# Kernel tuning notes

Measured on AMD Instinct MI355X. Metric: run time of the kernel, lower is better.

The kernel has to match this reference:

```python
import jax, jax.numpy as jnp
import numpy as np
from jax import lax

DIL_R = 2            # dilation_radius
K = 2 * DIL_R + 1    # 5x5 morphology kernel
FOCAL_ALPHA = 0.25
FOCAL_GAMMA = 2.0
BOUNDARY_W = 1.0
IGNORE_IDX = 250


def setup_inputs() -> dict:
    key = jax.random.key(0)
    k1, k2 = jax.random.split(key)
    pred = jax.random.normal(k1, (32, 2, 512, 512), dtype=jnp.float32)
    target = jax.random.randint(k2, (32, 512, 512), 0, 2, dtype=jnp.int64)
    return {"pred": pred, "target": target}


def _boundary_mask(target):
    # labels float, 5x5 all-ones conv with 'same' padding (zero pad),
    # dilated = (conv > 0), eroded = (-conv(-x) > K*K-1) == (conv(x) > K*K-1)
    x = target.astype(jnp.float32)[:, None]                    # [B,1,H,W]
    kern = jnp.ones((1, 1, K, K), dtype=jnp.float32)
    s = lax.conv_general_dilated(x, kern, (1, 1), 'SAME',
                                 dimension_numbers=('NCHW', 'OIHW', 'NCHW'))
    dilated = (s > 0).astype(jnp.float32)
    eroded = (s > (K * K - 1)).astype(jnp.float32)
    return (dilated - eroded)[:, 0]                            # [B,H,W]


def _loss(pred, target, boundary):
    logp = jax.nn.log_softmax(pred, axis=1)                    # [B,2,H,W]
    # per-pixel CE
    ce_pix = -jnp.take_along_axis(logp, target[:, None].astype(jnp.int32), axis=1)[:, 0]  # [B,H,W]
    # main CE with ignore_index=250
    valid = (target != IGNORE_IDX)
    ce_loss = jnp.sum(ce_pix * valid) / jnp.maximum(jnp.sum(valid), 1)
    # focal loss (no ignore, mean over all pixels)
    pt = jnp.exp(-ce_pix)
    focal = jnp.mean(FOCAL_ALPHA * (1.0 - pt) ** FOCAL_GAMMA * ce_pix)
    # boundary dice on class-1 prob
    prob1 = jnp.exp(logp[:, 1])                                # softmax(pred,1)[:,1]
    tgt_f = target.astype(jnp.float32)
    bp = prob1 * boundary
    bt = tgt_f * boundary
    inter = jnp.sum(bp * bt, axis=(1, 2))
    union = jnp.sum(bp, axis=(1, 2)) + jnp.sum(bt, axis=(1, 2))
    dice = 2.0 * inter / (union + 1e-8)
    bdice = 1.0 - jnp.mean(dice)
    return ce_loss + BOUNDARY_W * focal + BOUNDARY_W * bdice


def reference(pred, target):
    boundary = _boundary_mask(target)
    return _loss(pred, target, boundary)
```

## Files before the change

### kernel.cpp

```cpp
#include <hip/hip_runtime.h>
#include <math.h>

#define BATCH 32
#define HH 512
#define WW 512
#define TH 16
#define HALO 2
#define SRH (TH + 2*HALO)
#define NDW (WW / 4)
#define CSTRIDE 132
#define NPIX ((float)BATCH * HH * WW)
#define HW (HH * WW)
#define NBLK (BATCH * (HH / TH))


__global__ __launch_bounds__(256, 4) void bel_main_kernel(
        const float* __restrict__ pred,
        const int*   __restrict__ target,
        float*       __restrict__ ws) {
    __shared__ unsigned int t8[SRH][NDW];
    __shared__ unsigned int csum[TH][CSTRIDE];
    __shared__ float red[6][4];

    const int tid = threadIdx.x;
    const int bid = blockIdx.x;
    const int b   = bid >> 5;
    const int ty  = bid & 31;
    const int y0  = ty * TH;
    const size_t tb = (size_t)b * HW;

    if (tid < 2 * TH) {
        int rr = tid >> 1;
        csum[rr][(tid & 1) ? (NDW + 1) : 0] = 0u;
    }

    #pragma unroll
    for (int it = 0; it < (SRH * NDW) / 256; ++it) {
        const int i  = tid + 256 * it;
        const int r  = i >> 7;
        const int c4 = i & 127;
        const int gy = y0 - HALO + r;
        unsigned int packed = 0u;
        if ((unsigned)gy < (unsigned)HH) {
            const int4 v = *(const int4*)(target + tb + ((size_t)gy << 9) + (c4 << 2));
            packed = (unsigned)v.x | ((unsigned)v.y << 8)
                   | ((unsigned)v.z << 16) | ((unsigned)v.w << 24);
        }
        t8[r][c4] = packed;
    }
    __syncthreads();

    #pragma unroll
    for (int it = 0; it < (TH * NDW) / 256; ++it) {
        const int j = tid + 256 * it;
        const int r = j >> 7;
        const int c = j & 127;
        csum[r][c + 1] = t8[r][c] + t8[r+1][c] + t8[r+2][c]
                       + t8[r+3][c] + t8[r+4][c];
    }
    __syncthreads();

    const float4* __restrict__ pr0 = (const float4*)(pred + tb * 2);
    const float4* __restrict__ pr1 = (const float4*)(pred + tb * 2 + HW);
    const int base4 = (y0 << 7) + tid;

    float4 F0[8], F1[8];
    #pragma unroll
    for (int it = 0; it < 8; ++it) F0[it] = pr0[base4 + 256 * it];
    #pragma unroll
    for (int it = 0; it < 8; ++it) F1[it] = pr1[base4 + 256 * it];

    float ce_acc = 0.f, cnt_acc = 0.f, focal_acc = 0.f;
    float inter_acc = 0.f, bp_acc = 0.f, bt_acc = 0.f;

    const unsigned long long M5 = 0xFFFFFFFFFFull;
    const unsigned long long ALL5 = 0x0505050505ull;

    const int g  = tid & 127;
    const int rb = tid >> 7;

    #pragma unroll
    for (int it = 0; it < 8; ++it) {
        const int r = rb + 2 * it;

        const float4 f0 = F0[it];
        const float4 f1 = F1[it];

        const unsigned int L = csum[r][g];
        const unsigned int M = csum[r][g + 1];
        const unsigned int R = csum[r][g + 2];
        const unsigned int tdw = t8[r + HALO][g];

        const unsigned long long lo  = (unsigned long long)L | ((unsigned long long)M << 32);
        const unsigned long long mid = (unsigned long long)M | ((unsigned long long)R << 32);

        #pragma unroll
        for (int i = 0; i < 4; ++i) {
            unsigned long long w;
            if      (i == 0) w = (lo  >> 16) & M5;
            else if (i == 1) w = (lo  >> 24) & M5;
            else if (i == 2) w =  mid        & M5;
            else             w = (mid >>  8) & M5;
            const float bm = (w != 0ull && w != ALL5) ? 1.0f : 0.0f;

            const unsigned int tv = (tdw >> (8 * i)) & 0xFFu;

            const float p0 = (i == 0) ? f0.x : (i == 1) ? f0.y : (i == 2) ? f0.z : f0.w;
            const float p1 = (i == 0) ? f1.x : (i == 1) ? f1.y : (i == 2) ? f1.z : f1.w;

            const float d  = p1 - p0;
            const float e  = __expf(-fabsf(d));
            const float rz = 1.0f / (1.0f + e);
            const float pmin = e * rz;
            const float prob1 = (d >= 0.0f) ? rz : pmin;
            const float pt = tv ? prob1 : (1.0f - prob1);
            const float ce = -__logf(pt);

            const float valid = (tv != 250u) ? 1.0f : 0.0f;
            ce_acc  += ce * valid;
            cnt_acc += valid;

            const float omp = 1.0f - pt;
            focal_acc += omp * omp * ce;

            const float bp = prob1 * bm;
            const float bt = (float)tv * bm;
            inter_acc += bp * bt;
            bp_acc    += bp;
            bt_acc    += bt;
        }
    }

    float vals[6] = {ce_acc, cnt_acc, focal_acc * 0.25f, inter_acc, bp_acc, bt_acc};
    #pragma unroll
    for (int jj = 0; jj < 6; ++jj) {
        float v = vals[jj];
        #pragma unroll
        for (int off = 32; off > 0; off >>= 1)
            v += __shfl_down(v, off, 64);
        vals[jj] = v;
    }
    const int wave = tid >> 6;
    const int lane = tid & 63;
    if (lane == 0) {
        #pragma unroll
        for (int jj = 0; jj < 6; ++jj) red[jj][wave] = vals[jj];
    }
    __syncthreads();
    if (tid == 0) {
        float* p = ws + bid * 8;
        #pragma unroll
        for (int jj = 0; jj < 6; ++jj)
            p[jj] = red[jj][0] + red[jj][1] + red[jj][2] + red[jj][3];
    }
}

__global__ void bel_finalize_kernel(const float* __restrict__ ws,
                                    float* __restrict__ out) {
    __shared__ float simg[BATCH][4];
    const int t = threadIdx.x;
    const int b = t >> 3;
    const int s = t & 7;

    float a0 = 0.f, a1 = 0.f, a2 = 0.f, a3 = 0.f, a4 = 0.f, a5 = 0.f;
    #pragma unroll
    for (int k = 0; k < 4; ++k) {
        const int bid = (b << 5) + s + (k << 3);
        const float* p = ws + bid * 8;
        a0 += p[0]; a1 += p[1]; a2 += p[2];
        a3 += p[3]; a4 += p[4]; a5 += p[5];
    }
    #pragma unroll
    for (int off = 4; off > 0; off >>= 1) {
        a0 += __shfl_down(a0, off, 8);
        a1 += __shfl_down(a1, off, 8);
        a2 += __shfl_down(a2, off, 8);
        a3 += __shfl_down(a3, off, 8);
        a4 += __shfl_down(a4, off, 8);
        a5 += __shfl_down(a5, off, 8);
    }
    if (s == 0) {
        simg[b][0] = a0;
        simg[b][1] = a1;
        simg[b][2] = a2;
        simg[b][3] = 2.0f * a3 / (a4 + a5 + 1e-8f);
    }
    __syncthreads();
    if (t < BATCH) {
        float ce  = simg[t][0];
        float cnt = simg[t][1];
        float foc = simg[t][2];
        float dc  = simg[t][3];
        #pragma unroll
        for (int off = 16; off > 0; off >>= 1) {
            ce  += __shfl_down(ce,  off, 32);
            cnt += __shfl_down(cnt, off, 32);
            foc += __shfl_down(foc, off, 32);
            dc  += __shfl_down(dc,  off, 32);
        }
        if (t == 0) {
            const float ce_loss = ce / fmaxf(cnt, 1.0f);
            const float focal   = foc / NPIX;
            const float bdice   = 1.0f - dc / (float)BATCH;
            out[0] = ce_loss + focal + bdice;
        }
    }
}

extern "C" void kernel_launch(void* const* d_in, const int* in_sizes, int n_in,
                              void* d_out, int out_size, void* d_ws, size_t ws_size,
                              hipStream_t stream) {
    const float* pred   = (const float*)d_in[0];
    const int*   target = (const int*)d_in[1];
    float* ws  = (float*)d_ws;
    float* out = (float*)d_out;

    bel_main_kernel<<<NBLK, 256, 0, stream>>>(pred, target, ws);
    bel_finalize_kernel<<<1, 256, 0, stream>>>(ws, out);
}
```

Before: 117.5 us.

## Split fused kernel into boundary-map pass and prediction-loss pass

```diff
diff --git a/kernel.cpp b/kernel.cpp
--- a/kernel.cpp
+++ b/kernel.cpp
@@ -12,15 +12,15 @@
 #define NPIX ((float)BATCH * HH * WW)
 #define HW (HH * WW)
 #define NBLK (BATCH * (HH / TH))
-
-
-__global__ __launch_bounds__(256, 4) void bel_main_kernel(
-        const float* __restrict__ pred,
-        const int*   __restrict__ target,
-        float*       __restrict__ ws) {
+#define MAP_OFF 16384
+
+
+__global__ __launch_bounds__(256, 4) void bel_boundary_kernel(
+        const int* __restrict__ target,
+        float*     __restrict__ ws) {
     __shared__ unsigned int t8[SRH][NDW];
     __shared__ unsigned int csum[TH][CSTRIDE];
-    __shared__ float red[6][4];
+    __shared__ float red[2][4];
 
     const int tid = threadIdx.x;
     const int bid = blockIdx.x;
@@ -60,31 +60,18 @@
     }
     __syncthreads();
 
-    const float4* __restrict__ pr0 = (const float4*)(pred + tb * 2);
-    const float4* __restrict__ pr1 = (const float4*)(pred + tb * 2 + HW);
-    const int base4 = (y0 << 7) + tid;
-
-    float4 F0[8], F1[8];
-    #pragma unroll
-    for (int it = 0; it < 8; ++it) F0[it] = pr0[base4 + 256 * it];
-    #pragma unroll
-    for (int it = 0; it < 8; ++it) F1[it] = pr1[base4 + 256 * it];
-
-    float ce_acc = 0.f, cnt_acc = 0.f, focal_acc = 0.f;
-    float inter_acc = 0.f, bp_acc = 0.f, bt_acc = 0.f;
-
-    const unsigned long long M5 = 0xFFFFFFFFFFull;
+    unsigned int* __restrict__ mp = (unsigned int*)(ws + MAP_OFF);
+    const int mbase = b * (HW / 4) + (y0 << 7);
+
+    float cnt_acc = 0.f, bt_acc = 0.f;
+    const unsigned long long M5   = 0xFFFFFFFFFFull;
     const unsigned long long ALL5 = 0x0505050505ull;
-
     const int g  = tid & 127;
     const int rb = tid >> 7;
 
     #pragma unroll
     for (int it = 0; it < 8; ++it) {
         const int r = rb + 2 * it;
-
-        const float4 f0 = F0[it];
-        const float4 f1 = F1[it];
 
         const unsigned int L = csum[r][g];
         const unsigned int M = csum[r][g + 1];
@@ -94,6 +81,7 @@
         const unsigned long long lo  = (unsigned long long)L | ((unsigned long long)M << 32);
         const unsigned long long mid = (unsigned long long)M | ((unsigned long long)R << 32);
 
+        unsigned int codedw = 0u;
         #pragma unroll
         for (int i = 0; i < 4; ++i) {
             unsigned long long w;
@@ -101,9 +89,71 @@
             else if (i == 1) w = (lo  >> 24) & M5;
             else if (i == 2) w =  mid        & M5;
             else             w = (mid >>  8) & M5;
-            const float bm = (w != 0ull && w != ALL5) ? 1.0f : 0.0f;
-
+            const unsigned int bm = (w != 0ull && w != ALL5) ? 1u : 0u;
             const unsigned int tv = (tdw >> (8 * i)) & 0xFFu;
+
+            cnt_acc += (tv != 250u) ? 1.0f : 0.0f;
+            bt_acc  += (float)tv * (float)bm;
+
+            codedw |= ((tv & 1u) | (bm << 1)) << (8 * i);
+        }
+        mp[mbase + (r << 7) + g] = codedw;
+    }
+
+    float vals[2] = {cnt_acc, bt_acc};
+    #pragma unroll
+    for (int jj = 0; jj < 2; ++jj) {
+        float v = vals[jj];
+        #pragma unroll
+        for (int off = 32; off > 0; off >>= 1)
+            v += __shfl_down(v, off, 64);
+        vals[jj] = v;
+    }
+    const int wave = tid >> 6;
+    const int lane = tid & 63;
+    if (lane == 0) {
+        red[0][wave] = vals[0];
+        red[1][wave] = vals[1];
+    }
+    __syncthreads();
+    if (tid == 0) {
+        float* p = ws + bid * 16;
+        p[0] = red[0][0] + red[0][1] + red[0][2] + red[0][3];
+        p[1] = red[1][0] + red[1][1] + red[1][2] + red[1][3];
+    }
+}
+
+__global__ __launch_bounds__(256, 4) void bel_pred_kernel(
+        const float* __restrict__ pred,
+        float*       __restrict__ ws) {
+    __shared__ float red[4][4];
+
+    const int tid = threadIdx.x;
+    const int bid = blockIdx.x;
+    const int b   = bid >> 5;
+    const int ty  = bid & 31;
+    const int y0  = ty * TH;
+    const size_t tb = (size_t)b * HW;
+
+    const float4* __restrict__ pr0 = (const float4*)(pred + tb * 2);
+    const float4* __restrict__ pr1 = (const float4*)(pred + tb * 2 + HW);
+    const unsigned int* __restrict__ mp = (const unsigned int*)(ws + MAP_OFF);
+    const int base4 = (y0 << 7) + tid;
+    const int mbase = b * (HW / 4) + base4;
+
+    float ce_acc = 0.f, focal_acc = 0.f, inter_acc = 0.f, bp_acc = 0.f;
+
+    #pragma unroll
+    for (int it = 0; it < 8; ++it) {
+        const float4 f0 = pr0[base4 + 256 * it];
+        const float4 f1 = pr1[base4 + 256 * it];
+        const unsigned int cw = mp[mbase + 256 * it];
+
+        #pragma unroll
+        for (int i = 0; i < 4; ++i) {
+            const unsigned int code = (cw >> (8 * i)) & 0xFFu;
+            const float tv = (float)(code & 1u);
+            const float bm = (float)((code >> 1) & 1u);
 
             const float p0 = (i == 0) ? f0.x : (i == 1) ? f0.y : (i == 2) ? f0.z : f0.w;
             const float p1 = (i == 0) ? f1.x : (i == 1) ? f1.y : (i == 2) ? f1.z : f1.w;
@@ -113,27 +163,22 @@
             const float rz = 1.0f / (1.0f + e);
             const float pmin = e * rz;
             const float prob1 = (d >= 0.0f) ? rz : pmin;
-            const float pt = tv ? prob1 : (1.0f - prob1);
+            const float pt = (code & 1u) ? prob1 : (1.0f - prob1);
             const float ce = -__logf(pt);
 
-            const float valid = (tv != 250u) ? 1.0f : 0.0f;
-            ce_acc  += ce * valid;
-            cnt_acc += valid;
-
+            ce_acc += ce;
             const float omp = 1.0f - pt;
             focal_acc += omp * omp * ce;
 
             const float bp = prob1 * bm;
-            const float bt = (float)tv * bm;
-            inter_acc += bp * bt;
+            inter_acc += bp * tv;
             bp_acc    += bp;
-            bt_acc    += bt;
-        }
-    }
-
-    float vals[6] = {ce_acc, cnt_acc, focal_acc * 0.25f, inter_acc, bp_acc, bt_acc};
-    #pragma unroll
-    for (int jj = 0; jj < 6; ++jj) {
+        }
+    }
+
+    float vals[4] = {ce_acc, focal_acc * 0.25f, inter_acc, bp_acc};
+    #pragma unroll
+    for (int jj = 0; jj < 4; ++jj) {
         float v = vals[jj];
         #pragma unroll
         for (int off = 32; off > 0; off >>= 1)
@@ -144,13 +189,13 @@
     const int lane = tid & 63;
     if (lane == 0) {
         #pragma unroll
-        for (int jj = 0; jj < 6; ++jj) red[jj][wave] = vals[jj];
+        for (int jj = 0; jj < 4; ++jj) red[jj][wave] = vals[jj];
     }
     __syncthreads();
     if (tid == 0) {
-        float* p = ws + bid * 8;
-        #pragma unroll
-        for (int jj = 0; jj < 6; ++jj)
+        float* p = ws + bid * 16 + 8;
+        #pragma unroll
+        for (int jj = 0; jj < 4; ++jj)
             p[jj] = red[jj][0] + red[jj][1] + red[jj][2] + red[jj][3];
     }
 }
@@ -162,46 +207,47 @@
     const int b = t >> 3;
     const int s = t & 7;
 
-    float a0 = 0.f, a1 = 0.f, a2 = 0.f, a3 = 0.f, a4 = 0.f, a5 = 0.f;
+    float cnt = 0.f, bt = 0.f, ce = 0.f, foc = 0.f, inter = 0.f, bp = 0.f;
     #pragma unroll
     for (int k = 0; k < 4; ++k) {
         const int bid = (b << 5) + s + (k << 3);
-        const float* p = ws + bid * 8;
-        a0 += p[0]; a1 += p[1]; a2 += p[2];
-        a3 += p[3]; a4 += p[4]; a5 += p[5];
+        const float* p = ws + bid * 16;
+        cnt += p[0];  bt  += p[1];
+        ce  += p[8];  foc += p[9];
+        inter += p[10]; bp += p[11];
     }
     #pragma unroll
     for (int off = 4; off > 0; off >>= 1) {
-        a0 += __shfl_down(a0, off, 8);
-        a1 += __shfl_down(a1, off, 8);
-        a2 += __shfl_down(a2, off, 8);
-        a3 += __shfl_down(a3, off, 8);
-        a4 += __shfl_down(a4, off, 8);
-        a5 += __shfl_down(a5, off, 8);
+        cnt  += __shfl_down(cnt,  off, 8);
+        bt   += __shfl_down(bt,   off, 8);
+        ce   += __shfl_down(ce,   off, 8);
+        foc  += __shfl_down(foc,  off, 8);
+        inter+= __shfl_down(inter,off, 8);
+        bp   += __shfl_down(bp,   off, 8);
     }
     if (s == 0) {
-        simg[b][0] = a0;
-        simg[b][1] = a1;
-        simg[b][2] = a2;
-        simg[b][3] = 2.0f * a3 / (a4 + a5 + 1e-8f);
+        simg[b][0] = ce;
+        simg[b][1] = cnt;
+        simg[b][2] = foc;
+        simg[b][3] = 2.0f * inter / (bp + bt + 1e-8f);
     }
     __syncthreads();
     if (t < BATCH) {
-        float ce  = simg[t][0];
-        float cnt = simg[t][1];
-        float foc = simg[t][2];
-        float dc  = simg[t][3];
+        float a = simg[t][0];
+        float c = simg[t][1];
+        float f = simg[t][2];
+        float d = simg[t][3];
         #pragma unroll
         for (int off = 16; off > 0; off >>= 1) {
-            ce  += __shfl_down(ce,  off, 32);
-            cnt += __shfl_down(cnt, off, 32);
-            foc += __shfl_down(foc, off, 32);
-            dc  += __shfl_down(dc,  off, 32);
+            a += __shfl_down(a, off, 32);
+            c += __shfl_down(c, off, 32);
+            f += __shfl_down(f, off, 32);
+            d += __shfl_down(d, off, 32);
         }
         if (t == 0) {
-            const float ce_loss = ce / fmaxf(cnt, 1.0f);
-            const float focal   = foc / NPIX;
-            const float bdice   = 1.0f - dc / (float)BATCH;
+            const float ce_loss = a / fmaxf(c, 1.0f);
+            const float focal   = f / NPIX;
+            const float bdice   = 1.0f - d / (float)BATCH;
             out[0] = ce_loss + focal + bdice;
         }
     }
@@ -215,6 +261,7 @@
     float* ws  = (float*)d_ws;
     float* out = (float*)d_out;
 
-    bel_main_kernel<<<NBLK, 256, 0, stream>>>(pred, target, ws);
+    bel_boundary_kernel<<<NBLK, 256, 0, stream>>>(target, ws);
+    bel_pred_kernel<<<NBLK, 256, 0, stream>>>(pred, ws);
     bel_finalize_kernel<<<1, 256, 0, stream>>>(ws, out);
 }
```

Measured after the change: 124.9 us. +6.3%, slower.

## Replace shared-memory tile with per-wave register sliding window and lane shuffles

Applied to the files above, without the earlier changes.

```diff
diff --git a/kernel.cpp b/kernel.cpp
--- a/kernel.cpp
+++ b/kernel.cpp
@@ -4,95 +4,77 @@
 #define BATCH 32
 #define HH 512
 #define WW 512
-#define TH 16
-#define HALO 2
-#define SRH (TH + 2*HALO)
-#define NDW (WW / 4)
-#define CSTRIDE 132
+#define RS 8
 #define NPIX ((float)BATCH * HH * WW)
 #define HW (HH * WW)
-#define NBLK (BATCH * (HH / TH))
+#define NWAVE (BATCH * 2 * (HH / RS))
+#define NBLK (NWAVE / 4)
 
 
 __global__ __launch_bounds__(256, 4) void bel_main_kernel(
         const float* __restrict__ pred,
         const int*   __restrict__ target,
         float*       __restrict__ ws) {
-    __shared__ unsigned int t8[SRH][NDW];
-    __shared__ unsigned int csum[TH][CSTRIDE];
     __shared__ float red[6][4];
 
-    const int tid = threadIdx.x;
-    const int bid = blockIdx.x;
-    const int b   = bid >> 5;
-    const int ty  = bid & 31;
-    const int y0  = ty * TH;
-    const size_t tb = (size_t)b * HW;
-
-    if (tid < 2 * TH) {
-        int rr = tid >> 1;
-        csum[rr][(tid & 1) ? (NDW + 1) : 0] = 0u;
-    }
-
-    #pragma unroll
-    for (int it = 0; it < (SRH * NDW) / 256; ++it) {
-        const int i  = tid + 256 * it;
-        const int r  = i >> 7;
-        const int c4 = i & 127;
-        const int gy = y0 - HALO + r;
-        unsigned int packed = 0u;
-        if ((unsigned)gy < (unsigned)HH) {
-            const int4 v = *(const int4*)(target + tb + ((size_t)gy << 9) + (c4 << 2));
-            packed = (unsigned)v.x | ((unsigned)v.y << 8)
-                   | ((unsigned)v.z << 16) | ((unsigned)v.w << 24);
-        }
-        t8[r][c4] = packed;
-    }
-    __syncthreads();
-
-    #pragma unroll
-    for (int it = 0; it < (TH * NDW) / 256; ++it) {
-        const int j = tid + 256 * it;
-        const int r = j >> 7;
-        const int c = j & 127;
-        csum[r][c + 1] = t8[r][c] + t8[r+1][c] + t8[r+2][c]
-                       + t8[r+3][c] + t8[r+4][c];
-    }
-    __syncthreads();
-
-    const float4* __restrict__ pr0 = (const float4*)(pred + tb * 2);
-    const float4* __restrict__ pr1 = (const float4*)(pred + tb * 2 + HW);
-    const int base4 = (y0 << 7) + tid;
-
-    float4 F0[8], F1[8];
-    #pragma unroll
-    for (int it = 0; it < 8; ++it) F0[it] = pr0[base4 + 256 * it];
-    #pragma unroll
-    for (int it = 0; it < 8; ++it) F1[it] = pr1[base4 + 256 * it];
+    const int tid  = threadIdx.x;
+    const int lane = tid & 63;
+    const int wv   = (blockIdx.x << 2) + (tid >> 6);
+    const int b    = wv >> 7;
+    const int s    = wv & 127;
+    const int h    = s & 1;
+    const int y0   = (s >> 1) * RS;
+    const int cd   = (h << 6) + lane;
+
+    const int* __restrict__ tg = target + (size_t)b * HW;
+    const float4* __restrict__ pr0 = (const float4*)(pred + (size_t)b * 2 * HW);
+    const float4* __restrict__ pr1 = pr0 + (HW / 4);
+
+    const bool hasext = h ? (lane == 0) : (lane == 63);
+    const int  ecd    = h ? 63 : 64;
+
+    auto ldrow = [&](int r, int c) -> unsigned int {
+        if ((unsigned)r >= (unsigned)HH) return 0u;
+        const int4 v = *(const int4*)(tg + ((size_t)r << 9) + (c << 2));
+        return (unsigned)v.x | ((unsigned)v.y << 8)
+             | ((unsigned)v.z << 16) | ((unsigned)v.w << 24);
+    };
+
+    unsigned int w0 = ldrow(y0 - 2, cd);
+    unsigned int w1 = ldrow(y0 - 1, cd);
+    unsigned int w2 = ldrow(y0,     cd);
+    unsigned int w3 = ldrow(y0 + 1, cd);
+    unsigned int e0 = hasext ? ldrow(y0 - 2, ecd) : 0u;
+    unsigned int e1 = hasext ? ldrow(y0 - 1, ecd) : 0u;
+    unsigned int e2 = hasext ? ldrow(y0,     ecd) : 0u;
+    unsigned int e3 = hasext ? ldrow(y0 + 1, ecd) : 0u;
 
     float ce_acc = 0.f, cnt_acc = 0.f, focal_acc = 0.f;
     float inter_acc = 0.f, bp_acc = 0.f, bt_acc = 0.f;
 
-    const unsigned long long M5 = 0xFFFFFFFFFFull;
+    const unsigned long long M5   = 0xFFFFFFFFFFull;
     const unsigned long long ALL5 = 0x0505050505ull;
 
-    const int g  = tid & 127;
-    const int rb = tid >> 7;
-
-    #pragma unroll
-    for (int it = 0; it < 8; ++it) {
-        const int r = rb + 2 * it;
-
-        const float4 f0 = F0[it];
-        const float4 f1 = F1[it];
-
-        const unsigned int L = csum[r][g];
-        const unsigned int M = csum[r][g + 1];
-        const unsigned int R = csum[r][g + 2];
-        const unsigned int tdw = t8[r + HALO][g];
-
-        const unsigned long long lo  = (unsigned long long)L | ((unsigned long long)M << 32);
-        const unsigned long long mid = (unsigned long long)M | ((unsigned long long)R << 32);
+    #pragma unroll 2
+    for (int it = 0; it < RS; ++it) {
+        const int y = y0 + it;
+        const unsigned int w4 = ldrow(y + 2, cd);
+        const unsigned int e4 = hasext ? ldrow(y + 2, ecd) : 0u;
+
+        const float4 f0 = pr0[(y << 7) + cd];
+        const float4 f1 = pr1[(y << 7) + cd];
+
+        const unsigned int vs  = w0 + w1 + w2 + w3 + w4;
+        const unsigned int vse = e0 + e1 + e2 + e3 + e4;
+
+        unsigned int vsL = __shfl_up(vs, 1, 64);
+        unsigned int vsR = __shfl_down(vs, 1, 64);
+        vsL = (lane == 0)  ? vse : vsL;
+        vsR = (lane == 63) ? vse : vsR;
+
+        const unsigned long long lo  = (unsigned long long)vsL | ((unsigned long long)vs  << 32);
+        const unsigned long long mid = (unsigned long long)vs  | ((unsigned long long)vsR << 32);
+        const unsigned int tdw = w2;
 
         #pragma unroll
         for (int i = 0; i < 4; ++i) {
@@ -129,6 +111,9 @@
             bp_acc    += bp;
             bt_acc    += bt;
         }
+
+        w0 = w1; w1 = w2; w2 = w3; w3 = w4;
+        e0 = e1; e1 = e2; e2 = e3; e3 = e4;
     }
 
     float vals[6] = {ce_acc, cnt_acc, focal_acc * 0.25f, inter_acc, bp_acc, bt_acc};
@@ -141,14 +126,13 @@
         vals[jj] = v;
     }
     const int wave = tid >> 6;
-    const int lane = tid & 63;
-    if (lane == 0) {
+    if ((tid & 63) == 0) {
         #pragma unroll
         for (int jj = 0; jj < 6; ++jj) red[jj][wave] = vals[jj];
     }
     __syncthreads();
     if (tid == 0) {
-        float* p = ws + bid * 8;
+        float* p = ws + blockIdx.x * 8;
         #pragma unroll
         for (int jj = 0; jj < 6; ++jj)
             p[jj] = red[jj][0] + red[jj][1] + red[jj][2] + red[jj][3];
```

Measured after the change: 120.3 us. +2.4%, slower.
